# Performance work log

Hardware: AMD Instinct MI355X
Metric: run time of the kernel (lower is better)

Reference implementation:

```python
import jax, jax.numpy as jnp
import numpy as np

B, S, F_IN = 2048, 256, 3
COND = 4
EMBED = 4
HID = 64
NUM_CODES = 256
BETA = 0.25


def _linear_params(key, fan_in, fan_out):
    k1, k2 = jax.random.split(key)
    lim = 1.0 / np.sqrt(fan_in)
    w = jax.random.uniform(k1, (fan_in, fan_out), jnp.float32, -lim, lim)
    b = jax.random.uniform(k2, (fan_out,), jnp.float32, -lim, lim)
    return w, b


def setup_inputs() -> dict:
    key = jax.random.key(0)
    ks = jax.random.split(key, 10)
    x = jax.random.normal(ks[0], (B, S, F_IN), jnp.float32)
    mask = jnp.ones((B, S), jnp.float32)
    x_conditional = jax.random.normal(ks[1], (B, COND), jnp.float32)
    enc_w1, enc_b1 = _linear_params(ks[2], F_IN + COND, HID)
    enc_w2, enc_b2 = _linear_params(ks[3], HID, HID)
    enc_w3, enc_b3 = _linear_params(ks[4], HID, EMBED)
    codebook = jax.random.normal(ks[5], (NUM_CODES, EMBED), jnp.float32)
    dec_w1, dec_b1 = _linear_params(ks[6], EMBED + COND, HID)
    dec_w2, dec_b2 = _linear_params(ks[7], HID, HID)
    dec_w3, dec_b3 = _linear_params(ks[8], HID, F_IN)
    return dict(x=x, mask=mask, x_conditional=x_conditional,
                enc_w1=enc_w1, enc_b1=enc_b1, enc_w2=enc_w2, enc_b2=enc_b2,
                enc_w3=enc_w3, enc_b3=enc_b3, codebook=codebook,
                dec_w1=dec_w1, dec_b1=dec_b1, dec_w2=dec_w2, dec_b2=dec_b2,
                dec_w3=dec_w3, dec_b3=dec_b3)


def _mlp(x, w1, b1, w2, b2, w3, b3):
    h = jax.nn.relu(x @ w1 + b1)
    h = jax.nn.relu(h @ w2 + b2)
    return h @ w3 + b3


def _vq(z, codebook):
    # z: [B, S, E]; nearest-codebook assignment via expanded squared L2
    zf = z.reshape(-1, z.shape[-1])                       # [N, E]
    d = (jnp.sum(zf * zf, axis=-1, keepdims=True)
         - 2.0 * zf @ codebook.T
         + jnp.sum(codebook * codebook, axis=-1))         # [N, num_codes]
    idx = jnp.argmin(d, axis=-1)                          # [N]
    z_q = codebook[idx].reshape(z.shape)                  # [B, S, E]
    # VQ losses (codebook + beta * commitment)
    loss = (jnp.mean((jax.lax.stop_gradient(z) - z_q) ** 2)
            + BETA * jnp.mean((z - jax.lax.stop_gradient(z_q)) ** 2))
    # straight-through estimator
    z_q_st = z + jax.lax.stop_gradient(z_q - z)
    return z_q_st, loss, idx.reshape(z.shape[:-1])


def reference(x, mask, x_conditional,
              enc_w1, enc_b1, enc_w2, enc_b2, enc_w3, enc_b3,
              codebook,
              dec_w1, dec_b1, dec_w2, dec_b2, dec_w3, dec_b3):
    cond = jnp.broadcast_to(x_conditional[:, None, :], (B, S, COND))
    xin = jnp.concatenate([x, cond], axis=-1) * mask[..., None]
    z = _mlp(xin, enc_w1, enc_b1, enc_w2, enc_b2, enc_w3, enc_b3)
    z_q, vq_loss, idx = _vq(z, codebook)
    zdec = jnp.concatenate([z_q, cond], axis=-1) * mask[..., None]
    x_reco = _mlp(zdec, dec_w1, dec_b1, dec_w2, dec_b2, dec_w3, dec_b3)
    return x_reco, vq_loss, idx
```

## Files before the change

### kernel.cpp

```cpp
#include <hip/hip_runtime.h>
#include <hip/hip_bf16.h>

#define BB   2048
#define SS   256
#define NTOK (BB*SS)
#define FIN  3
#define CND  4
#define EMB  4
#define HID  64
#define NC   256
#define TPB  256

typedef __attribute__((ext_vector_type(16))) float f32x16;

#define OF_EW1T 0
#define OF_DW1T 512
#define OF_DB1  1024
#define OF_EW3  1088
#define OF_DW3T 1344
#define OF_CB   1600
#define OF_CC   2624
#define SMEM_F  2880

__global__ __launch_bounds__(TPB, 2) void vqvae_fused(
        const float* __restrict__ x, const float* __restrict__ mask,
        const float* __restrict__ cond,
        const float* __restrict__ ew1, const float* __restrict__ eb1,
        const float* __restrict__ ew2, const float* __restrict__ eb2,
        const float* __restrict__ ew3, const float* __restrict__ eb3,
        const float* __restrict__ cb,
        const float* __restrict__ dw1, const float* __restrict__ db1,
        const float* __restrict__ dw2, const float* __restrict__ db2,
        const float* __restrict__ dw3, const float* __restrict__ db3,
        float* __restrict__ out, float* __restrict__ loss_ws) {
    __shared__ float smem[SMEM_F];
    const int tid = threadIdx.x;

    for (int idx = tid; idx < (FIN+CND)*HID; idx += TPB) {
        int i = idx >> 6, j = idx & 63;
        smem[OF_EW1T + j*8 + i] = ew1[idx];
    }
    for (int j = tid; j < HID; j += TPB) smem[OF_EW1T + j*8 + 7] = eb1[j];
    for (int idx = tid; idx < (EMB+CND)*HID; idx += TPB) {
        int i = idx >> 6, j = idx & 63;
        smem[OF_DW1T + j*8 + i] = dw1[idx];
    }
    for (int j = tid; j < HID; j += TPB) smem[OF_DB1 + j] = db1[j];
    for (int i = tid; i < HID*EMB; i += TPB) smem[OF_EW3 + i] = ew3[i];
    for (int j = tid; j < HID; j += TPB) {
        smem[OF_DW3T + j*4 + 0] = dw3[j*FIN + 0];
        smem[OF_DW3T + j*4 + 1] = dw3[j*FIN + 1];
        smem[OF_DW3T + j*4 + 2] = dw3[j*FIN + 2];
        smem[OF_DW3T + j*4 + 3] = 0.0f;
    }
    for (int i = tid; i < NC*EMB; i += TPB) smem[OF_CB + i] = cb[i];
    {
        float c0 = cb[tid*EMB+0], c1 = cb[tid*EMB+1];
        float c2 = cb[tid*EMB+2], c3 = cb[tid*EMB+3];
        smem[OF_CC+tid] = ((c0*c0 + c1*c1) + c2*c2) + c3*c3;
    }
    __syncthreads();

    const int n0 = blockIdx.x * (2*TPB) + tid;
    const int n1 = n0 + TPB;
    const float m0 = mask[n0];
    const float m1 = mask[n1];
    const int bu0 = n0 >> 8;
    const int bu1 = bu0 + 1;

    float xin0[FIN+CND], xin1[FIN+CND];
    #pragma unroll
    for (int i = 0; i < FIN; i++) xin0[i] = x[n0*FIN + i] * m0;
    #pragma unroll
    for (int i = 0; i < FIN; i++) xin1[i] = x[n1*FIN + i] * m1;
    #pragma unroll
    for (int i = 0; i < CND; i++) xin0[FIN+i] = cond[bu0*CND + i] * m0;
    #pragma unroll
    for (int i = 0; i < CND; i++) xin1[FIN+i] = cond[bu1*CND + i] * m1;

    float hA[HID], hB[HID];
    #pragma unroll
    for (int j = 0; j < HID; j++) {
        float4 lo = *(const float4*)&smem[OF_EW1T + j*8 + 0];
        float4 hi = *(const float4*)&smem[OF_EW1T + j*8 + 4];
        float a = xin0[0] * lo.x;
        float b = xin1[0] * lo.x;
        a = fmaf(xin0[1], lo.y, a);  b = fmaf(xin1[1], lo.y, b);
        a = fmaf(xin0[2], lo.z, a);  b = fmaf(xin1[2], lo.z, b);
        a = fmaf(xin0[3], lo.w, a);  b = fmaf(xin1[3], lo.w, b);
        a = fmaf(xin0[4], hi.x, a);  b = fmaf(xin1[4], hi.x, b);
        a = fmaf(xin0[5], hi.y, a);  b = fmaf(xin1[5], hi.y, b);
        a = fmaf(xin0[6], hi.z, a);  b = fmaf(xin1[6], hi.z, b);
        hA[j] = fmaxf(a + hi.w, 0.0f);
        hB[j] = fmaxf(b + hi.w, 0.0f);
    }

    float z0 = 0.f, z1 = 0.f, z2 = 0.f, z3 = 0.f;
    float y0 = 0.f, y1 = 0.f, y2 = 0.f, y3 = 0.f;
    for (int jt = 0; jt < 4; jt++) {
        float a[16], b[16];
        #pragma unroll
        for (int u = 0; u < 16; u++) { a[u] = 0.f; b[u] = 0.f; }
        #pragma unroll
        for (int k = 0; k < HID; k++) {
            f32x16 w = *(const f32x16*)&ew2[k*HID + jt*16];
            #pragma unroll
            for (int u = 0; u < 16; u++) {
                a[u] = fmaf(hA[k], w[u], a[u]);
                b[u] = fmaf(hB[k], w[u], b[u]);
            }
        }
        f32x16 bb = *(const f32x16*)&eb2[jt*16];
        #pragma unroll
        for (int u = 0; u < 16; u++) {
            float ta = fmaxf(a[u] + bb[u], 0.0f);
            float tb = fmaxf(b[u] + bb[u], 0.0f);
            float4 w3 = *(const float4*)&smem[OF_EW3 + (jt*16+u)*EMB];
            z0 = fmaf(ta, w3.x, z0); z1 = fmaf(ta, w3.y, z1);
            z2 = fmaf(ta, w3.z, z2); z3 = fmaf(ta, w3.w, z3);
            y0 = fmaf(tb, w3.x, y0); y1 = fmaf(tb, w3.y, y1);
            y2 = fmaf(tb, w3.z, y2); y3 = fmaf(tb, w3.w, y3);
        }
    }
    z0 += eb3[0]; z1 += eb3[1];
    z2 += eb3[2]; z3 += eb3[3];
    y0 += eb3[0]; y1 += eb3[1];
    y2 += eb3[2]; y3 += eb3[3];

    const float zzA = ((z0*z0 + z1*z1) + z2*z2) + z3*z3;
    const float zzB = ((y0*y0 + y1*y1) + y2*y2) + y3*y3;
    float bestA = 3.4e38f, bestB = 3.4e38f;
    int   biA = 0, biB = 0;
    #pragma unroll 4
    for (int ci = 0; ci < NC; ci++) {
        float4 c = *(const float4*)&smem[OF_CB + ci*EMB];
        float cc = smem[OF_CC + ci];
        float dotA = z0 * c.x;
        dotA = fmaf(z1, c.y, dotA);
        dotA = fmaf(z2, c.z, dotA);
        dotA = fmaf(z3, c.w, dotA);
        float dA = (zzA - 2.0f*dotA) + cc;
        if (dA < bestA) { bestA = dA; biA = ci; }
        float dotB = y0 * c.x;
        dotB = fmaf(y1, c.y, dotB);
        dotB = fmaf(y2, c.z, dotB);
        dotB = fmaf(y3, c.w, dotB);
        float dB = (zzB - 2.0f*dotB) + cc;
        if (dB < bestB) { bestB = dB; biB = ci; }
    }
    float4 qA = *(const float4*)&smem[OF_CB + biA*EMB];
    float4 qB = *(const float4*)&smem[OF_CB + biB*EMB];

    float e0 = z0-qA.x, e1 = z1-qA.y, e2 = z2-qA.z, e3 = z3-qA.w;
    float f0 = y0-qB.x, f1 = y1-qB.y, f2 = y2-qB.z, f3 = y3-qB.w;
    float sq = (((e0*e0 + e1*e1) + e2*e2) + e3*e3)
             + (((f0*f0 + f1*f1) + f2*f2) + f3*f3);
    #pragma unroll
    for (int off = 32; off > 0; off >>= 1) sq += __shfl_down(sq, off, 64);
    if ((tid & 63) == 0) atomicAdd(loss_ws, sq);

    out[NTOK*FIN + 1 + n0] = (float)biA;
    out[NTOK*FIN + 1 + n1] = (float)biB;

    float zd0[EMB+CND], zd1[EMB+CND];
    zd0[0] = qA.x*m0; zd0[1] = qA.y*m0; zd0[2] = qA.z*m0; zd0[3] = qA.w*m0;
    zd1[0] = qB.x*m1; zd1[1] = qB.y*m1; zd1[2] = qB.z*m1; zd1[3] = qB.w*m1;
    #pragma unroll
    for (int i = 0; i < CND; i++) zd0[EMB+i] = cond[bu0*CND + i] * m0;
    #pragma unroll
    for (int i = 0; i < CND; i++) zd1[EMB+i] = cond[bu1*CND + i] * m1;

    #pragma unroll
    for (int j = 0; j < HID; j++) {
        float4 lo = *(const float4*)&smem[OF_DW1T + j*8 + 0];
        float4 hi = *(const float4*)&smem[OF_DW1T + j*8 + 4];
        float a = zd0[0] * lo.x;
        float b = zd1[0] * lo.x;
        a = fmaf(zd0[1], lo.y, a);  b = fmaf(zd1[1], lo.y, b);
        a = fmaf(zd0[2], lo.z, a);  b = fmaf(zd1[2], lo.z, b);
        a = fmaf(zd0[3], lo.w, a);  b = fmaf(zd1[3], lo.w, b);
        a = fmaf(zd0[4], hi.x, a);  b = fmaf(zd1[4], hi.x, b);
        a = fmaf(zd0[5], hi.y, a);  b = fmaf(zd1[5], hi.y, b);
        a = fmaf(zd0[6], hi.z, a);  b = fmaf(zd1[6], hi.z, b);
        a = fmaf(zd0[7], hi.w, a);  b = fmaf(zd1[7], hi.w, b);
        float bias = smem[OF_DB1 + j];
        hA[j] = fmaxf(a + bias, 0.0f);
        hB[j] = fmaxf(b + bias, 0.0f);
    }

    float r0 = 0.f, r1 = 0.f, r2 = 0.f;
    float s0 = 0.f, s1 = 0.f, s2 = 0.f;
    for (int jt = 0; jt < 4; jt++) {
        float a[16], b[16];
        #pragma unroll
        for (int u = 0; u < 16; u++) { a[u] = 0.f; b[u] = 0.f; }
        #pragma unroll
        for (int k = 0; k < HID; k++) {
            f32x16 w = *(const f32x16*)&dw2[k*HID + jt*16];
            #pragma unroll
            for (int u = 0; u < 16; u++) {
                a[u] = fmaf(hA[k], w[u], a[u]);
                b[u] = fmaf(hB[k], w[u], b[u]);
            }
        }
        f32x16 bb = *(const f32x16*)&db2[jt*16];
        #pragma unroll
        for (int u = 0; u < 16; u++) {
            float ta = fmaxf(a[u] + bb[u], 0.0f);
            float tb = fmaxf(b[u] + bb[u], 0.0f);
            float4 w = *(const float4*)&smem[OF_DW3T + (jt*16+u)*4];
            r0 = fmaf(ta, w.x, r0); s0 = fmaf(tb, w.x, s0);
            r1 = fmaf(ta, w.y, r1); s1 = fmaf(tb, w.y, s1);
            r2 = fmaf(ta, w.z, r2); s2 = fmaf(tb, w.z, s2);
        }
    }
    r0 += db3[0]; r1 += db3[1]; r2 += db3[2];
    s0 += db3[0]; s1 += db3[1]; s2 += db3[2];

    out[n0*FIN + 0] = r0;
    out[n0*FIN + 1] = r1;
    out[n0*FIN + 2] = r2;
    out[n1*FIN + 0] = s0;
    out[n1*FIN + 1] = s1;
    out[n1*FIN + 2] = s2;
}

__global__ void finalize_kernel(float* out, const float* loss_ws) {
    out[NTOK*FIN] = 1.25f * loss_ws[0] * (1.0f / (float)(NTOK*EMB));
}

extern "C" void kernel_launch(void* const* d_in, const int* in_sizes, int n_in,
                              void* d_out, int out_size, void* d_ws, size_t ws_size,
                              hipStream_t stream) {
    (void)in_sizes; (void)n_in; (void)ws_size; (void)out_size;
    float* ws = (float*)d_ws;
    hipMemsetAsync(ws, 0, sizeof(float), stream);

    vqvae_fused<<<NTOK/(2*TPB), TPB, 0, stream>>>(
        (const float*)d_in[0], (const float*)d_in[1], (const float*)d_in[2],
        (const float*)d_in[3], (const float*)d_in[4], (const float*)d_in[5],
        (const float*)d_in[6], (const float*)d_in[7], (const float*)d_in[8],
        (const float*)d_in[9], (const float*)d_in[10], (const float*)d_in[11],
        (const float*)d_in[12], (const float*)d_in[13], (const float*)d_in[14],
        (const float*)d_in[15],
        (float*)d_out, ws);

    finalize_kernel<<<1, 1, 0, stream>>>((float*)d_out, ws);
}
```

Before: 284.1 us.

## Process four tokens per thread with packed f32x2 math and LDS-staged weights

Each thread now handles four tokens instead of two, packed into two-wide float vectors so the compiler can emit packed FMA instructions (v_pk_fma_f32 on CDNA). The 64x64 hidden weights and biases are staged into shared memory, replacing wide scalar global loads from ew2/dw2 with LDS float4 reads. Output-tile width per inner loop drops from 16 to 4 to make room in registers for the four-token state. Register pressure and occupancy may suffer, and the grid halves to 512 blocks, which could underfill the GPU.

```diff
diff --git a/kernel.cpp b/kernel.cpp
--- a/kernel.cpp
+++ b/kernel.cpp
@@ -11,16 +11,21 @@
 #define NC   256
 #define TPB  256
 
-typedef __attribute__((ext_vector_type(16))) float f32x16;
+typedef __attribute__((ext_vector_type(2))) float f32x2;
+#define Z2 ((f32x2){0.0f, 0.0f})
 
 #define OF_EW1T 0
 #define OF_DW1T 512
 #define OF_DB1  1024
-#define OF_EW3  1088
-#define OF_DW3T 1344
-#define OF_CB   1600
-#define OF_CC   2624
-#define SMEM_F  2880
+#define OF_EB2  1088
+#define OF_DB2  1152
+#define OF_EW3  1216
+#define OF_DW3T 1472
+#define OF_CB   1728
+#define OF_CC   2752
+#define OF_EW2F 3008
+#define OF_DW2F 7104
+#define SMEM_F  11200
 
 __global__ __launch_bounds__(TPB, 2) void vqvae_fused(
         const float* __restrict__ x, const float* __restrict__ mask,
@@ -46,6 +51,8 @@
         smem[OF_DW1T + j*8 + i] = dw1[idx];
     }
     for (int j = tid; j < HID; j += TPB) smem[OF_DB1 + j] = db1[j];
+    for (int j = tid; j < HID; j += TPB) smem[OF_EB2 + j] = eb2[j];
+    for (int j = tid; j < HID; j += TPB) smem[OF_DB2 + j] = db2[j];
     for (int i = tid; i < HID*EMB; i += TPB) smem[OF_EW3 + i] = ew3[i];
     for (int j = tid; j < HID; j += TPB) {
         smem[OF_DW3T + j*4 + 0] = dw3[j*FIN + 0];
@@ -54,6 +61,10 @@
         smem[OF_DW3T + j*4 + 3] = 0.0f;
     }
     for (int i = tid; i < NC*EMB; i += TPB) smem[OF_CB + i] = cb[i];
+    for (int i = tid; i < HID*HID/4; i += TPB) {
+        *(float4*)&smem[OF_EW2F + i*4] = *(const float4*)&ew2[i*4];
+        *(float4*)&smem[OF_DW2F + i*4] = *(const float4*)&dw2[i*4];
+    }
     {
         float c0 = cb[tid*EMB+0], c1 = cb[tid*EMB+1];
         float c2 = cb[tid*EMB+2], c3 = cb[tid*EMB+3];
@@ -61,168 +72,227 @@
     }
     __syncthreads();
 
-    const int n0 = blockIdx.x * (2*TPB) + tid;
+    const int n0 = blockIdx.x * (4*TPB) + tid;
     const int n1 = n0 + TPB;
-    const float m0 = mask[n0];
-    const float m1 = mask[n1];
+    const int n2 = n0 + 2*TPB;
+    const int n3 = n0 + 3*TPB;
+    const float m0 = mask[n0], m1 = mask[n1], m2 = mask[n2], m3 = mask[n3];
     const int bu0 = n0 >> 8;
-    const int bu1 = bu0 + 1;
-
-    float xin0[FIN+CND], xin1[FIN+CND];
-    #pragma unroll
-    for (int i = 0; i < FIN; i++) xin0[i] = x[n0*FIN + i] * m0;
-    #pragma unroll
-    for (int i = 0; i < FIN; i++) xin1[i] = x[n1*FIN + i] * m1;
-    #pragma unroll
-    for (int i = 0; i < CND; i++) xin0[FIN+i] = cond[bu0*CND + i] * m0;
-    #pragma unroll
-    for (int i = 0; i < CND; i++) xin1[FIN+i] = cond[bu1*CND + i] * m1;
-
-    float hA[HID], hB[HID];
+    const int bu1 = bu0 + 1, bu2 = bu0 + 2, bu3 = bu0 + 3;
+
+    f32x2 xinAB[FIN+CND], xinCD[FIN+CND];
+    #pragma unroll
+    for (int i = 0; i < FIN; i++) {
+        xinAB[i] = (f32x2){x[n0*FIN + i] * m0, x[n1*FIN + i] * m1};
+        xinCD[i] = (f32x2){x[n2*FIN + i] * m2, x[n3*FIN + i] * m3};
+    }
+    #pragma unroll
+    for (int i = 0; i < CND; i++) {
+        xinAB[FIN+i] = (f32x2){cond[bu0*CND + i] * m0, cond[bu1*CND + i] * m1};
+        xinCD[FIN+i] = (f32x2){cond[bu2*CND + i] * m2, cond[bu3*CND + i] * m3};
+    }
+
+    f32x2 hAB[HID], hCD[HID];
     #pragma unroll
     for (int j = 0; j < HID; j++) {
         float4 lo = *(const float4*)&smem[OF_EW1T + j*8 + 0];
         float4 hi = *(const float4*)&smem[OF_EW1T + j*8 + 4];
-        float a = xin0[0] * lo.x;
-        float b = xin1[0] * lo.x;
-        a = fmaf(xin0[1], lo.y, a);  b = fmaf(xin1[1], lo.y, b);
-        a = fmaf(xin0[2], lo.z, a);  b = fmaf(xin1[2], lo.z, b);
-        a = fmaf(xin0[3], lo.w, a);  b = fmaf(xin1[3], lo.w, b);
-        a = fmaf(xin0[4], hi.x, a);  b = fmaf(xin1[4], hi.x, b);
-        a = fmaf(xin0[5], hi.y, a);  b = fmaf(xin1[5], hi.y, b);
-        a = fmaf(xin0[6], hi.z, a);  b = fmaf(xin1[6], hi.z, b);
-        hA[j] = fmaxf(a + hi.w, 0.0f);
-        hB[j] = fmaxf(b + hi.w, 0.0f);
-    }
-
-    float z0 = 0.f, z1 = 0.f, z2 = 0.f, z3 = 0.f;
-    float y0 = 0.f, y1 = 0.f, y2 = 0.f, y3 = 0.f;
-    for (int jt = 0; jt < 4; jt++) {
-        float a[16], b[16];
-        #pragma unroll
-        for (int u = 0; u < 16; u++) { a[u] = 0.f; b[u] = 0.f; }
+        f32x2 a = xinAB[0] * lo.x;
+        f32x2 c = xinCD[0] * lo.x;
+        a = xinAB[1]*lo.y + a;  c = xinCD[1]*lo.y + c;
+        a = xinAB[2]*lo.z + a;  c = xinCD[2]*lo.z + c;
+        a = xinAB[3]*lo.w + a;  c = xinCD[3]*lo.w + c;
+        a = xinAB[4]*hi.x + a;  c = xinCD[4]*hi.x + c;
+        a = xinAB[5]*hi.y + a;  c = xinCD[5]*hi.y + c;
+        a = xinAB[6]*hi.z + a;  c = xinCD[6]*hi.z + c;
+        f32x2 ta = a + hi.w, tc = c + hi.w;
+        hAB[j] = (f32x2){fmaxf(ta.x, 0.0f), fmaxf(ta.y, 0.0f)};
+        hCD[j] = (f32x2){fmaxf(tc.x, 0.0f), fmaxf(tc.y, 0.0f)};
+    }
+
+    f32x2 z0AB = Z2, z1AB = Z2, z2AB = Z2, z3AB = Z2;
+    f32x2 z0CD = Z2, z1CD = Z2, z2CD = Z2, z3CD = Z2;
+    for (int jt = 0; jt < 16; jt++) {
+        f32x2 a0 = Z2, a1 = Z2, a2 = Z2, a3 = Z2;
+        f32x2 c0 = Z2, c1 = Z2, c2 = Z2, c3 = Z2;
         #pragma unroll
         for (int k = 0; k < HID; k++) {
-            f32x16 w = *(const f32x16*)&ew2[k*HID + jt*16];
-            #pragma unroll
-            for (int u = 0; u < 16; u++) {
-                a[u] = fmaf(hA[k], w[u], a[u]);
-                b[u] = fmaf(hB[k], w[u], b[u]);
-            }
+            float4 w = *(const float4*)&smem[OF_EW2F + k*HID + jt*4];
+            f32x2 hab = hAB[k], hcd = hCD[k];
+            a0 = hab*w.x + a0;  a1 = hab*w.y + a1;
+            a2 = hab*w.z + a2;  a3 = hab*w.w + a3;
+            c0 = hcd*w.x + c0;  c1 = hcd*w.y + c1;
+            c2 = hcd*w.z + c2;  c3 = hcd*w.w + c3;
         }
-        f32x16 bb = *(const f32x16*)&eb2[jt*16];
-        #pragma unroll
-        for (int u = 0; u < 16; u++) {
-            float ta = fmaxf(a[u] + bb[u], 0.0f);
-            float tb = fmaxf(b[u] + bb[u], 0.0f);
-            float4 w3 = *(const float4*)&smem[OF_EW3 + (jt*16+u)*EMB];
-            z0 = fmaf(ta, w3.x, z0); z1 = fmaf(ta, w3.y, z1);
-            z2 = fmaf(ta, w3.z, z2); z3 = fmaf(ta, w3.w, z3);
-            y0 = fmaf(tb, w3.x, y0); y1 = fmaf(tb, w3.y, y1);
-            y2 = fmaf(tb, w3.z, y2); y3 = fmaf(tb, w3.w, y3);
-        }
-    }
-    z0 += eb3[0]; z1 += eb3[1];
-    z2 += eb3[2]; z3 += eb3[3];
-    y0 += eb3[0]; y1 += eb3[1];
-    y2 += eb3[2]; y3 += eb3[3];
-
-    const float zzA = ((z0*z0 + z1*z1) + z2*z2) + z3*z3;
-    const float zzB = ((y0*y0 + y1*y1) + y2*y2) + y3*y3;
-    float bestA = 3.4e38f, bestB = 3.4e38f;
-    int   biA = 0, biB = 0;
-    #pragma unroll 4
+        float4 bb = *(const float4*)&smem[OF_EB2 + jt*4];
+        f32x2 s0 = a0 + bb.x, s1 = a1 + bb.y, s2 = a2 + bb.z, s3 = a3 + bb.w;
+        f32x2 u0 = c0 + bb.x, u1 = c1 + bb.y, u2 = c2 + bb.z, u3 = c3 + bb.w;
+        f32x2 ta0 = (f32x2){fmaxf(s0.x,0.f), fmaxf(s0.y,0.f)};
+        f32x2 ta1 = (f32x2){fmaxf(s1.x,0.f), fmaxf(s1.y,0.f)};
+        f32x2 ta2 = (f32x2){fmaxf(s2.x,0.f), fmaxf(s2.y,0.f)};
+        f32x2 ta3 = (f32x2){fmaxf(s3.x,0.f), fmaxf(s3.y,0.f)};
+        f32x2 tc0 = (f32x2){fmaxf(u0.x,0.f), fmaxf(u0.y,0.f)};
+        f32x2 tc1 = (f32x2){fmaxf(u1.x,0.f), fmaxf(u1.y,0.f)};
+        f32x2 tc2 = (f32x2){fmaxf(u2.x,0.f), fmaxf(u2.y,0.f)};
+        f32x2 tc3 = (f32x2){fmaxf(u3.x,0.f), fmaxf(u3.y,0.f)};
+        float4 w0 = *(const float4*)&smem[OF_EW3 + (jt*4+0)*EMB];
+        z0AB = ta0*w0.x + z0AB; z1AB = ta0*w0.y + z1AB;
+        z2AB = ta0*w0.z + z2AB; z3AB = ta0*w0.w + z3AB;
+        z0CD = tc0*w0.x + z0CD; z1CD = tc0*w0.y + z1CD;
+        z2CD = tc0*w0.z + z2CD; z3CD = tc0*w0.w + z3CD;
+        float4 w1 = *(const float4*)&smem[OF_EW3 + (jt*4+1)*EMB];
+        z0AB = ta1*w1.x + z0AB; z1AB = ta1*w1.y + z1AB;
+        z2AB = ta1*w1.z + z2AB; z3AB = ta1*w1.w + z3AB;
+        z0CD = tc1*w1.x + z0CD; z1CD = tc1*w1.y + z1CD;
+        z2CD = tc1*w1.z + z2CD; z3CD = tc1*w1.w + z3CD;
+        float4 w2 = *(const float4*)&smem[OF_EW3 + (jt*4+2)*EMB];
+        z0AB = ta2*w2.x + z0AB; z1AB = ta2*w2.y + z1AB;
+        z2AB = ta2*w2.z + z2AB; z3AB = ta2*w2.w + z3AB;
+        z0CD = tc2*w2.x + z0CD; z1CD = tc2*w2.y + z1CD;
+        z2CD = tc2*w2.z + z2CD; z3CD = tc2*w2.w + z3CD;
+        float4 w3 = *(const float4*)&smem[OF_EW3 + (jt*4+3)*EMB];
+        z0AB = ta3*w3.x + z0AB; z1AB = ta3*w3.y + z1AB;
+        z2AB = ta3*w3.z + z2AB; z3AB = ta3*w3.w + z3AB;
+        z0CD = tc3*w3.x + z0CD; z1CD = tc3*w3.y + z1CD;
+        z2CD = tc3*w3.z + z2CD; z3CD = tc3*w3.w + z3CD;
+    }
+    z0AB = z0AB + eb3[0]; z1AB = z1AB + eb3[1];
+    z2AB = z2AB + eb3[2]; z3AB = z3AB + eb3[3];
+    z0CD = z0CD + eb3[0]; z1CD = z1CD + eb3[1];
+    z2CD = z2CD + eb3[2]; z3CD = z3CD + eb3[3];
+
+    const f32x2 zzAB = ((z0AB*z0AB + z1AB*z1AB) + z2AB*z2AB) + z3AB*z3AB;
+    const f32x2 zzCD = ((z0CD*z0CD + z1CD*z1CD) + z2CD*z2CD) + z3CD*z3CD;
+    float bestA = 3.4e38f, bestB = 3.4e38f, bestC = 3.4e38f, bestD = 3.4e38f;
+    int   biA = 0, biB = 0, biC = 0, biD = 0;
+    #pragma unroll 2
     for (int ci = 0; ci < NC; ci++) {
         float4 c = *(const float4*)&smem[OF_CB + ci*EMB];
         float cc = smem[OF_CC + ci];
-        float dotA = z0 * c.x;
-        dotA = fmaf(z1, c.y, dotA);
-        dotA = fmaf(z2, c.z, dotA);
-        dotA = fmaf(z3, c.w, dotA);
-        float dA = (zzA - 2.0f*dotA) + cc;
-        if (dA < bestA) { bestA = dA; biA = ci; }
-        float dotB = y0 * c.x;
-        dotB = fmaf(y1, c.y, dotB);
-        dotB = fmaf(y2, c.z, dotB);
-        dotB = fmaf(y3, c.w, dotB);
-        float dB = (zzB - 2.0f*dotB) + cc;
-        if (dB < bestB) { bestB = dB; biB = ci; }
+        f32x2 dotAB = z0AB * c.x;
+        dotAB = z1AB*c.y + dotAB;
+        dotAB = z2AB*c.z + dotAB;
+        dotAB = z3AB*c.w + dotAB;
+        f32x2 dAB = (zzAB - 2.0f*dotAB) + cc;
+        if (dAB.x < bestA) { bestA = dAB.x; biA = ci; }
+        if (dAB.y < bestB) { bestB = dAB.y; biB = ci; }
+        f32x2 dotCD = z0CD * c.x;
+        dotCD = z1CD*c.y + dotCD;
+        dotCD = z2CD*c.z + dotCD;
+        dotCD = z3CD*c.w + dotCD;
+        f32x2 dCD = (zzCD - 2.0f*dotCD) + cc;
+        if (dCD.x < bestC) { bestC = dCD.x; biC = ci; }
+        if (dCD.y < bestD) { bestD = dCD.y; biD = ci; }
     }
     float4 qA = *(const float4*)&smem[OF_CB + biA*EMB];
     float4 qB = *(const float4*)&smem[OF_CB + biB*EMB];
-
-    float e0 = z0-qA.x, e1 = z1-qA.y, e2 = z2-qA.z, e3 = z3-qA.w;
-    float f0 = y0-qB.x, f1 = y1-qB.y, f2 = y2-qB.z, f3 = y3-qB.w;
-    float sq = (((e0*e0 + e1*e1) + e2*e2) + e3*e3)
-             + (((f0*f0 + f1*f1) + f2*f2) + f3*f3);
-    #pragma unroll
-    for (int off = 32; off > 0; off >>= 1) sq += __shfl_down(sq, off, 64);
-    if ((tid & 63) == 0) atomicAdd(loss_ws, sq);
+    float4 qC = *(const float4*)&smem[OF_CB + biC*EMB];
+    float4 qD = *(const float4*)&smem[OF_CB + biD*EMB];
+
+    {
+        float e0 = z0AB.x-qA.x, e1 = z1AB.x-qA.y, e2 = z2AB.x-qA.z, e3 = z3AB.x-qA.w;
+        float f0 = z0AB.y-qB.x, f1 = z1AB.y-qB.y, f2 = z2AB.y-qB.z, f3 = z3AB.y-qB.w;
+        float g0 = z0CD.x-qC.x, g1 = z1CD.x-qC.y, g2 = z2CD.x-qC.z, g3 = z3CD.x-qC.w;
+        float h0 = z0CD.y-qD.x, h1 = z1CD.y-qD.y, h2 = z2CD.y-qD.z, h3 = z3CD.y-qD.w;
+        float sq = (((e0*e0 + e1*e1) + e2*e2) + e3*e3)
+                 + (((f0*f0 + f1*f1) + f2*f2) + f3*f3)
+                 + (((g0*g0 + g1*g1) + g2*g2) + g3*g3)
+                 + (((h0*h0 + h1*h1) + h2*h2) + h3*h3);
+        #pragma unroll
+        for (int off = 32; off > 0; off >>= 1) sq += __shfl_down(sq, off, 64);
+        if ((tid & 63) == 0) atomicAdd(loss_ws, sq);
+    }
 
     out[NTOK*FIN + 1 + n0] = (float)biA;
     out[NTOK*FIN + 1 + n1] = (float)biB;
-
-    float zd0[EMB+CND], zd1[EMB+CND];
-    zd0[0] = qA.x*m0; zd0[1] = qA.y*m0; zd0[2] = qA.z*m0; zd0[3] = qA.w*m0;
-    zd1[0] = qB.x*m1; zd1[1] = qB.y*m1; zd1[2] = qB.z*m1; zd1[3] = qB.w*m1;
-    #pragma unroll
-    for (int i = 0; i < CND; i++) zd0[EMB+i] = cond[bu0*CND + i] * m0;
-    #pragma unroll
-    for (int i = 0; i < CND; i++) zd1[EMB+i] = cond[bu1*CND + i] * m1;
+    out[NTOK*FIN + 1 + n2] = (float)biC;
+    out[NTOK*FIN + 1 + n3] = (float)biD;
+
+    f32x2 zdAB[EMB+CND], zdCD[EMB+CND];
+    zdAB[0] = (f32x2){qA.x*m0, qB.x*m1};
+    zdAB[1] = (f32x2){qA.y*m0, qB.y*m1};
+    zdAB[2] = (f32x2){qA.z*m0, qB.z*m1};
+    zdAB[3] = (f32x2){qA.w*m0, qB.w*m1};
+    zdCD[0] = (f32x2){qC.x*m2, qD.x*m3};
+    zdCD[1] = (f32x2){qC.y*m2, qD.y*m3};
+    zdCD[2] = (f32x2){qC.z*m2, qD.z*m3};
+    zdCD[3] = (f32x2){qC.w*m2, qD.w*m3};
+    #pragma unroll
+    for (int i = 0; i < CND; i++) {
+        zdAB[EMB+i] = (f32x2){cond[bu0*CND + i] * m0, cond[bu1*CND + i] * m1};
+        zdCD[EMB+i] = (f32x2){cond[bu2*CND + i] * m2, cond[bu3*CND + i] * m3};
+    }
 
     #pragma unroll
     for (int j = 0; j < HID; j++) {
         float4 lo = *(const float4*)&smem[OF_DW1T + j*8 + 0];
         float4 hi = *(const float4*)&smem[OF_DW1T + j*8 + 4];
-        float a = zd0[0] * lo.x;
-        float b = zd1[0] * lo.x;
-        a = fmaf(zd0[1], lo.y, a);  b = fmaf(zd1[1], lo.y, b);
-        a = fmaf(zd0[2], lo.z, a);  b = fmaf(zd1[2], lo.z, b);
-        a = fmaf(zd0[3], lo.w, a);  b = fmaf(zd1[3], lo.w, b);
-        a = fmaf(zd0[4], hi.x, a);  b = fmaf(zd1[4], hi.x, b);
-        a = fmaf(zd0[5], hi.y, a);  b = fmaf(zd1[5], hi.y, b);
-        a = fmaf(zd0[6], hi.z, a);  b = fmaf(zd1[6], hi.z, b);
-        a = fmaf(zd0[7], hi.w, a);  b = fmaf(zd1[7], hi.w, b);
+        f32x2 a = zdAB[0] * lo.x;
+        f32x2 c = zdCD[0] * lo.x;
+        a = zdAB[1]*lo.y + a;  c = zdCD[1]*lo.y + c;
+        a = zdAB[2]*lo.z + a;  c = zdCD[2]*lo.z + c;
+        a = zdAB[3]*lo.w + a;  c = zdCD[3]*lo.w + c;
+        a = zdAB[4]*hi.x + a;  c = zdCD[4]*hi.x + c;
+        a = zdAB[5]*hi.y + a;  c = zdCD[5]*hi.y + c;
+        a = zdAB[6]*hi.z + a;  c = zdCD[6]*hi.z + c;
+        a = zdAB[7]*hi.w + a;  c = zdCD[7]*hi.w + c;
         float bias = smem[OF_DB1 + j];
-        hA[j] = fmaxf(a + bias, 0.0f);
-        hB[j] = fmaxf(b + bias, 0.0f);
-    }
-
-    float r0 = 0.f, r1 = 0.f, r2 = 0.f;
-    float s0 = 0.f, s1 = 0.f, s2 = 0.f;
-    for (int jt = 0; jt < 4; jt++) {
-        float a[16], b[16];
-        #pragma unroll
-        for (int u = 0; u < 16; u++) { a[u] = 0.f; b[u] = 0.f; }
+        f32x2 ta = a + bias, tc = c + bias;
+        hAB[j] = (f32x2){fmaxf(ta.x, 0.0f), fmaxf(ta.y, 0.0f)};
+        hCD[j] = (f32x2){fmaxf(tc.x, 0.0f), fmaxf(tc.y, 0.0f)};
+    }
+
+    f32x2 rAB0 = Z2, rAB1 = Z2, rAB2 = Z2;
+    f32x2 rCD0 = Z2, rCD1 = Z2, rCD2 = Z2;
+    for (int jt = 0; jt < 16; jt++) {
+        f32x2 a0 = Z2, a1 = Z2, a2 = Z2, a3 = Z2;
+        f32x2 c0 = Z2, c1 = Z2, c2 = Z2, c3 = Z2;
         #pragma unroll
         for (int k = 0; k < HID; k++) {
-            f32x16 w = *(const f32x16*)&dw2[k*HID + jt*16];
-            #pragma unroll
-            for (int u = 0; u < 16; u++) {
-                a[u] = fmaf(hA[k], w[u], a[u]);
-                b[u] = fmaf(hB[k], w[u], b[u]);
-            }
+            float4 w = *(const float4*)&smem[OF_DW2F + k*HID + jt*4];
+            f32x2 hab = hAB[k], hcd = hCD[k];
+            a0 = hab*w.x + a0;  a1 = hab*w.y + a1;
+            a2 = hab*w.z + a2;  a3 = hab*w.w + a3;
+            c0 = hcd*w.x + c0;  c1 = hcd*w.y + c1;
+            c2 = hcd*w.z + c2;  c3 = hcd*w.w + c3;
         }
-        f32x16 bb = *(const f32x16*)&db2[jt*16];
+        float4 bb = *(const float4*)&smem[OF_DB2 + jt*4];
+        f32x2 s0 = a0 + bb.x, s1 = a1 + bb.y, s2 = a2 + bb.z, s3 = a3 + bb.w;
+        f32x2 u0 = c0 + bb.x, u1 = c1 + bb.y, u2 = c2 + bb.z, u3 = c3 + bb.w;
+        f32x2 ta0 = (f32x2){fmaxf(s0.x,0.f), fmaxf(s0.y,0.f)};
+        f32x2 ta1 = (f32x2){fmaxf(s1.x,0.f), fmaxf(s1.y,0.f)};
+        f32x2 ta2 = (f32x2){fmaxf(s2.x,0.f), fmaxf(s2.y,0.f)};
+        f32x2 ta3 = (f32x2){fmaxf(s3.x,0.f), fmaxf(s3.y,0.f)};
+        f32x2 tc0 = (f32x2){fmaxf(u0.x,0.f), fmaxf(u0.y,0.f)};
+        f32x2 tc1 = (f32x2){fmaxf(u1.x,0.f), fmaxf(u1.y,0.f)};
+        f32x2 tc2 = (f32x2){fmaxf(u2.x,0.f), fmaxf(u2.y,0.f)};
+        f32x2 tc3 = (f32x2){fmaxf(u3.x,0.f), fmaxf(u3.y,0.f)};
         #pragma unroll
-        for (int u = 0; u < 16; u++) {
-            float ta = fmaxf(a[u] + bb[u], 0.0f);
-            float tb = fmaxf(b[u] + bb[u], 0.0f);
-            float4 w = *(const float4*)&smem[OF_DW3T + (jt*16+u)*4];
-            r0 = fmaf(ta, w.x, r0); s0 = fmaf(tb, w.x, s0);
-            r1 = fmaf(ta, w.y, r1); s1 = fmaf(tb, w.y, s1);
-            r2 = fmaf(ta, w.z, r2); s2 = fmaf(tb, w.z, s2);
+        for (int jj = 0; jj < 4; jj++) {
+            f32x2 ta = (jj==0)?ta0:(jj==1)?ta1:(jj==2)?ta2:ta3;
+            f32x2 tc = (jj==0)?tc0:(jj==1)?tc1:(jj==2)?tc2:tc3;
+            int j = jt*4 + jj;
+            float4 w = *(const float4*)&smem[OF_DW3T + j*4];
+            rAB0 = ta*w.x + rAB0;  rCD0 = tc*w.x + rCD0;
+            rAB1 = ta*w.y + rAB1;  rCD1 = tc*w.y + rCD1;
+            rAB2 = ta*w.z + rAB2;  rCD2 = tc*w.z + rCD2;
         }
     }
-    r0 += db3[0]; r1 += db3[1]; r2 += db3[2];
-    s0 += db3[0]; s1 += db3[1]; s2 += db3[2];
-
-    out[n0*FIN + 0] = r0;
-    out[n0*FIN + 1] = r1;
-    out[n0*FIN + 2] = r2;
-    out[n1*FIN + 0] = s0;
-    out[n1*FIN + 1] = s1;
-    out[n1*FIN + 2] = s2;
+    rAB0 = rAB0 + db3[0]; rAB1 = rAB1 + db3[1]; rAB2 = rAB2 + db3[2];
+    rCD0 = rCD0 + db3[0]; rCD1 = rCD1 + db3[1]; rCD2 = rCD2 + db3[2];
+
+    out[n0*FIN + 0] = rAB0.x;
+    out[n0*FIN + 1] = rAB1.x;
+    out[n0*FIN + 2] = rAB2.x;
+    out[n1*FIN + 0] = rAB0.y;
+    out[n1*FIN + 1] = rAB1.y;
+    out[n1*FIN + 2] = rAB2.y;
+    out[n2*FIN + 0] = rCD0.x;
+    out[n2*FIN + 1] = rCD1.x;
+    out[n2*FIN + 2] = rCD2.x;
+    out[n3*FIN + 0] = rCD0.y;
+    out[n3*FIN + 1] = rCD1.y;
+    out[n3*FIN + 2] = rCD2.y;
 }
 
 __global__ void finalize_kernel(float* out, const float* loss_ws) {
@@ -236,7 +306,7 @@
     float* ws = (float*)d_ws;
     hipMemsetAsync(ws, 0, sizeof(float), stream);
 
-    vqvae_fused<<<NTOK/(2*TPB), TPB, 0, stream>>>(
+    vqvae_fused<<<NTOK/(4*TPB), TPB, 0, stream>>>(
         (const float*)d_in[0], (const float*)d_in[1], (const float*)d_in[2],
         (const float*)d_in[3], (const float*)d_in[4], (const float*)d_in[5],
         (const float*)d_in[6], (const float*)d_in[7], (const float*)d_in[8],
```

Result: slower. 332.1 us (+16.9%).
